# Performance work log

Hardware: AMD Instinct MI355X
Metric: run time of the kernel (lower is better)

Reference implementation:

```python
import jax, jax.numpy as jnp
import numpy as np

B, L, D, H, MLP = 8, 1024, 768, 12, 3072
DH = D // H
EPS = 1e-5


def setup_inputs() -> dict:
    key = jax.random.key(0)
    ks = jax.random.split(key, 8)
    s = 0.02
    return {
        "x": jax.random.normal(ks[0], (B, L, D), dtype=jnp.float32),
        "ln1_g": jnp.ones((D,), jnp.float32),
        "ln1_b": jnp.zeros((D,), jnp.float32),
        "w_qkv": jax.random.normal(ks[1], (3 * D, D), dtype=jnp.float32) * s,
        "w_out": jax.random.normal(ks[2], (D, D), dtype=jnp.float32) * s,
        "b_out": jnp.zeros((D,), jnp.float32),
        "ln2_g": jnp.ones((D,), jnp.float32),
        "ln2_b": jnp.zeros((D,), jnp.float32),
        "w1": jax.random.normal(ks[3], (MLP, D), dtype=jnp.float32) * s,
        "b1": jnp.zeros((MLP,), jnp.float32),
        "w2": jax.random.normal(ks[4], (D, MLP), dtype=jnp.float32) * s,
        "b2": jnp.zeros((D,), jnp.float32),
    }


def _layernorm(x, g, b):
    mu = jnp.mean(x, axis=-1, keepdims=True)
    var = jnp.mean(jnp.square(x - mu), axis=-1, keepdims=True)
    return (x - mu) * jax.lax.rsqrt(var + EPS) * g + b


def reference(x, ln1_g, ln1_b, w_qkv, w_out, b_out, ln2_g, ln2_b, w1, b1, w2, b2):
    # --- self-attention branch ---
    xn = _layernorm(x, ln1_g, ln1_b)                     # [B, L, D]
    qkv = jnp.einsum('bld,ed->ble', xn, w_qkv)           # [B, L, 3D]
    # rearrange 'b l (qkv h d) -> qkv b h l d'
    qkv = qkv.reshape(B, L, 3, H, DH).transpose(2, 0, 3, 1, 4)
    q, k, v = qkv[0], qkv[1], qkv[2]                     # [B, H, L, DH]
    scale = DH ** -0.5
    att = jnp.einsum('bhxd,bhyd->bhxy', q, k) * scale    # [B, H, L, L]
    att = jax.nn.softmax(att, axis=-1)
    o = jnp.einsum('bhxy,bhyd->bhxd', att, v)            # [B, H, L, DH]
    o = o.transpose(0, 2, 1, 3).reshape(B, L, D)         # 'b h l d -> b l (h d)'
    o = jnp.einsum('bld,ed->ble', o, w_out) + b_out
    x = x + o
    # --- MLP branch ---
    xn = _layernorm(x, ln2_g, ln2_b)
    h = jax.nn.gelu(jnp.einsum('bld,md->blm', xn, w1) + b1, approximate=False)
    h = jnp.einsum('blm,dm->bld', h, w2) + b2
    return x + h
```

## Files before the change

kernel.cpp:

```cpp
#include <hip/hip_runtime.h>
#include <hip/hip_bf16.h>
#include <math.h>

#define NB 8
#define NL 1024
#define ND 768
#define NH 12
#define NDH 64
#define NMLP 3072
#define NROWS 8192

typedef __attribute__((ext_vector_type(8))) short short8;
typedef __attribute__((ext_vector_type(8))) __bf16 bf16x8;
typedef __attribute__((ext_vector_type(4))) float f32x4;
typedef __attribute__((ext_vector_type(4))) float float4v;
typedef __attribute__((ext_vector_type(4))) unsigned short ushort4v;

__device__ __forceinline__ unsigned short f2b(float f) {
  unsigned u = __float_as_uint(f);
  unsigned r = (u + 0x7fffu + ((u >> 16) & 1u)) >> 16;
  return (unsigned short)r;
}

__device__ __forceinline__ f32x4 mfma16(short8 a, short8 b, f32x4 c) {
  return __builtin_amdgcn_mfma_f32_16x16x32_bf16(
      __builtin_bit_cast(bf16x8, a), __builtin_bit_cast(bf16x8, b), c, 0, 0, 0);
}

__device__ __forceinline__ void gl_lds16(const void* g, void* l) {
  __builtin_amdgcn_global_load_lds(
      (__attribute__((address_space(1))) void*)g,
      (__attribute__((address_space(3))) void*)l, 16, 0, 0);
}

__global__ __launch_bounds__(256) void cvt_all(const float* __restrict__ s0,
                                               const float* __restrict__ s1,
                                               const float* __restrict__ s2,
                                               const float* __restrict__ s3,
                                               unsigned short* __restrict__ d) {
  int i = (blockIdx.x * 256 + threadIdx.x) * 4;
  const float* s;
  int off;
  if (i < 1769472) { s = s0; off = i; }
  else if (i < 2359296) { s = s1; off = i - 1769472; }
  else if (i < 4718592) { s = s2; off = i - 2359296; }
  else { s = s3; off = i - 4718592; }
  float4v v = *(const float4v*)(s + off);
  ushort4v o;
  o[0] = f2b(v[0]); o[1] = f2b(v[1]); o[2] = f2b(v[2]); o[3] = f2b(v[3]);
  *(ushort4v*)(d + i) = o;
}

__global__ __launch_bounds__(256) void ln_bf16(const float* __restrict__ x,
                                               const float* __restrict__ g,
                                               const float* __restrict__ b,
                                               unsigned short* __restrict__ out) {
  int row = blockIdx.x, tid = threadIdx.x;
  const float* xr = x + (size_t)row * ND;
  float v0 = xr[tid], v1 = xr[tid + 256], v2 = xr[tid + 512];
  float s = v0 + v1 + v2;
  __shared__ float red[8];
#pragma unroll
  for (int o = 32; o > 0; o >>= 1) s += __shfl_down(s, o);
  int wv = tid >> 6, ln = tid & 63;
  if (ln == 0) red[wv] = s;
  __syncthreads();
  float mu = (red[0] + red[1] + red[2] + red[3]) * (1.0f / 768.0f);
  float d0 = v0 - mu, d1 = v1 - mu, d2 = v2 - mu;
  float q = d0 * d0 + d1 * d1 + d2 * d2;
#pragma unroll
  for (int o = 32; o > 0; o >>= 1) q += __shfl_down(q, o);
  if (ln == 0) red[4 + wv] = q;
  __syncthreads();
  float var = (red[4] + red[5] + red[6] + red[7]) * (1.0f / 768.0f);
  float rs = rsqrtf(var + 1e-5f);
  unsigned short* orow = out + (size_t)row * ND;
  orow[tid]       = f2b(d0 * rs * g[tid]       + b[tid]);
  orow[tid + 256] = f2b(d1 * rs * g[tid + 256] + b[tid + 256]);
  orow[tid + 512] = f2b(d2 * rs * g[tid + 512] + b[tid + 512]);
}

template <int MODE>
__global__ __launch_bounds__(256) void gemm_bt(
    const unsigned short* __restrict__ A, const unsigned short* __restrict__ W,
    unsigned short* __restrict__ outB, const float* __restrict__ bias,
    int M, int N, int K, int gx) {
  __shared__ __attribute__((aligned(16))) unsigned short As[3 * 4096];
  __shared__ __attribute__((aligned(16))) unsigned short Bs[3 * 4096];

  const int nwg = gridDim.x;
  const int bid = blockIdx.x;
  const int q = nwg >> 3, r = nwg & 7;
  const int xcd = bid & 7, idx = bid >> 3;
  const int swz = (xcd < r ? xcd * (q + 1) : r * (q + 1) + (xcd - r) * q) + idx;
  const int by = swz / gx, bx = swz - by * gx;
  const int m0 = by * 128, n0 = bx * 128;

  const int tid = threadIdx.x;
  const int wave = tid >> 6, lane = tid & 63;
  const int l15 = lane & 15, lhi = lane >> 4;
  const int wm = wave >> 1, wn = wave & 1;

  const int sr = tid >> 2, sc8 = (tid & 3) * 8;
  const unsigned short* Ag0 = A + (size_t)(m0 + sr) * K + sc8;
  const unsigned short* Ag1 = Ag0 + (size_t)64 * K;
  const unsigned short* Wg0 = W + (size_t)(n0 + sr) * K + sc8;
  const unsigned short* Wg1 = Wg0 + (size_t)64 * K;

  f32x4 acc[4][4];
#pragma unroll
  for (int i = 0; i < 4; i++)
#pragma unroll
    for (int j = 0; j < 4; j++) acc[i][j] = (f32x4){0.f, 0.f, 0.f, 0.f};

  auto STAGE = [&](int kelem, int buf) {
    unsigned short* Ad = As + buf * 4096 + wave * 512;
    unsigned short* Bd = Bs + buf * 4096 + wave * 512;
    gl_lds16(Ag0 + kelem, Ad);
    gl_lds16(Ag1 + kelem, Ad + 2048);
    gl_lds16(Wg0 + kelem, Bd);
    gl_lds16(Wg1 + kelem, Bd + 2048);
  };

  const int NT = K >> 5;
  STAGE(0, 0);
  STAGE(32, 1);

  int cb = 0, nbuf = 2;
  for (int t = 0; t < NT; ++t) {
    if (t + 2 < NT) {
      STAGE((t + 2) * 32, nbuf);
      asm volatile("s_waitcnt vmcnt(8)" ::: "memory");
    } else if (t + 2 == NT) {
      asm volatile("s_waitcnt vmcnt(4)" ::: "memory");
    } else {
      asm volatile("s_waitcnt vmcnt(0)" ::: "memory");
    }
    __builtin_amdgcn_s_barrier();

    const unsigned short* Ac = As + cb * 4096;
    const unsigned short* Bc = Bs + cb * 4096;
    short8 af[4], bf[4];
#pragma unroll
    for (int i = 0; i < 4; i++)
      af[i] = *(const short8*)&Ac[(wm * 64 + i * 16 + l15) * 32 + lhi * 8];
#pragma unroll
    for (int j = 0; j < 4; j++)
      bf[j] = *(const short8*)&Bc[(wn * 64 + j * 16 + l15) * 32 + lhi * 8];
#pragma unroll
    for (int i = 0; i < 4; i++)
#pragma unroll
      for (int j = 0; j < 4; j++) acc[i][j] = mfma16(af[i], bf[j], acc[i][j]);

    asm volatile("s_waitcnt lgkmcnt(0)" ::: "memory");
    __builtin_amdgcn_s_barrier();
    cb = (cb == 2) ? 0 : cb + 1;
    nbuf = (nbuf == 2) ? 0 : nbuf + 1;
  }

#pragma unroll
  for (int i = 0; i < 4; i++) {
    int row = m0 + wm * 64 + i * 16 + lhi * 4;
#pragma unroll
    for (int j = 0; j < 4; j++) {
      int col = n0 + wn * 64 + j * 16 + l15;
#pragma unroll
      for (int r2 = 0; r2 < 4; r2++) {
        float v = acc[i][j][r2];
        size_t idxo = (size_t)(row + r2) * N + col;
        if (MODE == 0) {
          outB[idxo] = f2b(v);
        } else {
          float t2 = v + bias[col];
          float z = 1.5957691f * t2 * (1.0f + 0.044715f * t2 * t2);
          float e = __expf(-z);
          outB[idxo] = f2b(__fdividef(t2, 1.0f + e));
        }
      }
    }
  }
}

template <int MODE>
__global__ __launch_bounds__(256) void gemm_bt64(
    const unsigned short* __restrict__ A, const unsigned short* __restrict__ W,
    float* __restrict__ outF, const float* __restrict__ bias,
    const float* __restrict__ resid, int M, int N, int K, int gx) {
  __shared__ __attribute__((aligned(16))) unsigned short As[2 * 4096];
  __shared__ __attribute__((aligned(16))) unsigned short Bs[2 * 8192];

  const int nwg = gridDim.x;
  const int bid = blockIdx.x;
  const int q = nwg >> 3, r = nwg & 7;
  const int xcd = bid & 7, idx = bid >> 3;
  const int swz = (xcd < r ? xcd * (q + 1) : r * (q + 1) + (xcd - r) * q) + idx;
  const int by = swz / gx, bx = swz - by * gx;
  const int m0 = by * 64, n0 = bx * 128;

  const int tid = threadIdx.x;
  const int wave = tid >> 6, lane = tid & 63;
  const int l15 = lane & 15, lhi = lane >> 4;
  const int wn = wave;

  const int sr = tid >> 3;
  const int swc8 = ((tid & 7) ^ (sr & 7)) * 8;
  const unsigned short* Aga = A + (size_t)(m0 + sr) * K + swc8;
  const unsigned short* Wga = W + (size_t)(n0 + sr) * K + swc8;

  f32x4 acc[4][2];
#pragma unroll
  for (int i = 0; i < 4; i++)
#pragma unroll
    for (int j = 0; j < 2; j++) acc[i][j] = (f32x4){0.f, 0.f, 0.f, 0.f};

  auto STAGE = [&](int kelem, int buf) {
    unsigned short* Ad = As + buf * 4096 + wave * 512;
    unsigned short* Bd = Bs + buf * 8192 + wave * 512;
    gl_lds16(Aga + kelem, Ad);
    gl_lds16(Aga + (size_t)32 * K + kelem, Ad + 2048);
    gl_lds16(Wga + kelem, Bd);
    gl_lds16(Wga + (size_t)32 * K + kelem, Bd + 2048);
    gl_lds16(Wga + (size_t)64 * K + kelem, Bd + 4096);
    gl_lds16(Wga + (size_t)96 * K + kelem, Bd + 6144);
  };

  const int NT = K >> 6;
  STAGE(0, 0);

  for (int t = 0; t < NT; ++t) {
    const int cb = t & 1;
    if (t + 1 < NT) {
      STAGE((t + 1) * 64, cb ^ 1);
      asm volatile("s_waitcnt vmcnt(6)" ::: "memory");
    } else {
      asm volatile("s_waitcnt vmcnt(0)" ::: "memory");
    }
    __builtin_amdgcn_s_barrier();

    const unsigned short* Ac = As + cb * 4096;
    const unsigned short* Bc = Bs + cb * 8192;
    short8 af[4][2], bf[2][2];
#pragma unroll
    for (int i = 0; i < 4; i++) {
      int ar = i * 16 + l15;
#pragma unroll
      for (int kk = 0; kk < 2; kk++)
        af[i][kk] = *(const short8*)&Ac[ar * 64 + (((kk * 4 + lhi) ^ (ar & 7)) * 8)];
    }
#pragma unroll
    for (int j = 0; j < 2; j++) {
      int br = wn * 32 + j * 16 + l15;
#pragma unroll
      for (int kk = 0; kk < 2; kk++)
        bf[j][kk] = *(const short8*)&Bc[br * 64 + (((kk * 4 + lhi) ^ (br & 7)) * 8)];
    }
#pragma unroll
    for (int kk = 0; kk < 2; kk++)
#pragma unroll
      for (int i = 0; i < 4; i++)
#pragma unroll
        for (int j = 0; j < 2; j++)
          acc[i][j] = mfma16(af[i][kk], bf[j][kk], acc[i][j]);

    asm volatile("s_waitcnt lgkmcnt(0)" ::: "memory");
    __builtin_amdgcn_s_barrier();
  }

#pragma unroll
  for (int i = 0; i < 4; i++) {
    int row = m0 + i * 16 + lhi * 4;
#pragma unroll
    for (int j = 0; j < 2; j++) {
      int col = n0 + wn * 32 + j * 16 + l15;
#pragma unroll
      for (int r2 = 0; r2 < 4; r2++) {
        size_t idxo = (size_t)(row + r2) * N + col;
        outF[idxo] = acc[i][j][r2] + bias[col] + resid[idxo];
      }
    }
  }
}

__global__ __launch_bounds__(256) void vtrans(const unsigned short* __restrict__ qkv,
                                              unsigned short* __restrict__ vT) {
  int bid = blockIdx.x;
  int tt = bid & 15;
  int t2 = bid >> 4;
  int h = t2 % NH, b = t2 / NH;
  __shared__ unsigned short L[64 * 72];
  int t = threadIdx.x;
  int row0 = t >> 3;
  int col8 = (t & 7) * 8;
#pragma unroll
  for (int s = 0; s < 2; s++) {
    int row = row0 + s * 32;
    const unsigned short* src =
        qkv + ((size_t)(b * NL + tt * 64 + row)) * 2304 + 1536 + h * 64 + col8;
    short8 v = *(const short8*)src;
    int wchunk = row >> 3;
#pragma unroll
    for (int j = 0; j < 8; j++) {
      int d = col8 + j;
      int cp = wchunk ^ (d >> 3);
      L[d * 72 + cp * 8 + (row & 7)] = (unsigned short)v[j];
    }
  }
  __syncthreads();
#pragma unroll
  for (int s = 0; s < 2; s++) {
    int d = (t >> 3) + s * 32;
    int rc = t & 7;
    int cp = rc ^ (d >> 3);
    short8 ov = *(const short8*)&L[d * 72 + cp * 8];
    *(short8*)(vT + ((size_t)((b * NH + h) * 64 + d)) * NL + tt * 64 + rc * 8) = ov;
  }
}

#define L2E8 0.180336880f
__global__ __launch_bounds__(256, 3) void attn_kernel(
    const unsigned short* __restrict__ qkv, const unsigned short* __restrict__ vT,
    unsigned short* __restrict__ o) {
  int bid0 = blockIdx.x;
  int lb = (bid0 & 7) * 96 + (bid0 >> 3);
  int qt = lb & 7;
  int t = lb >> 3;
  int h = t % NH, b = t / NH;
  const int tid = threadIdx.x;
  const int wave = tid >> 6, lane = tid & 63;
  const int l15 = lane & 15, lhi = lane >> 4;
  const int sw = l15 & 7;
  __shared__ __attribute__((aligned(16))) unsigned short Ks[2 * 64 * 64];
  __shared__ __attribute__((aligned(16))) unsigned short Vs[2 * 64 * 64];
  __shared__ __attribute__((aligned(16))) unsigned short Ps[2 * 4 * 16 * 64];

  const unsigned short* qp = qkv + (size_t)(b * NL + qt * 128) * 2304 + h * 64;
  short8 qf[2][2];
#pragma unroll
  for (int i = 0; i < 2; i++)
#pragma unroll
    for (int kk = 0; kk < 2; kk++)
      qf[i][kk] = *(const short8*)(qp + (size_t)(i * 64 + wave * 16 + l15) * 2304 +
                                   kk * 32 + lhi * 8);

  const int srow = tid >> 3, scpos = tid & 7;
  const int sc8 = (scpos ^ (srow & 7)) * 8;
  const unsigned short* ks0 =
      qkv + (size_t)(b * NL + srow) * 2304 + 768 + h * 64 + sc8;
  const unsigned short* vt0 =
      vT + (size_t)((b * NH + h) * 64 + srow) * NL + sc8;
  unsigned short* Pw0 = Ps + wave * 1024;
  unsigned short* Pw1 = Ps + 4096 + wave * 1024;

  int paddr[4][4];
#pragma unroll
  for (int kb = 0; kb < 4; kb++) {
    int ch = kb * 2 + (l15 >> 3);
#pragma unroll
    for (int r = 0; r < 4; r++) {
      int row = lhi * 4 + r;
      paddr[kb][r] = row * 64 + ((ch ^ (row & 7)) << 3) + sw;
    }
  }

  f32x4 acc[2][4];
  f32x4 accL[2];
#pragma unroll
  for (int i = 0; i < 2; i++) {
    accL[i] = (f32x4){0.f, 0.f, 0.f, 0.f};
#pragma unroll
    for (int nb = 0; nb < 4; nb++) acc[i][nb] = (f32x4){0.f, 0.f, 0.f, 0.f};
  }

  short8 onesf;
#pragma unroll
  for (int j = 0; j < 8; j++) onesf[j] = (short)0x3F80;

#define STAGE(ktile, buf)                                                    \
  {                                                                          \
    const unsigned short* ksrc = ks0 + (size_t)((ktile) * 64) * 2304;        \
    const unsigned short* vsrc = vt0 + (ktile) * 64;                         \
    unsigned short* kb_ = Ks + (buf) * 4096 + wave * 512;                    \
    unsigned short* vb_ = Vs + (buf) * 4096 + wave * 512;                    \
    gl_lds16(ksrc, kb_);                                                     \
    gl_lds16(ksrc + (size_t)32 * 2304, kb_ + 2048);                          \
    gl_lds16(vsrc, vb_);                                                     \
    gl_lds16(vsrc + 32 * NL, vb_ + 2048);                                    \
  }

  STAGE(0, 0);

  for (int kt = 0; kt < 16; kt++) {
    const int cb = kt & 1;
    if (kt + 1 < 16) {
      STAGE(kt + 1, cb ^ 1);
      asm volatile("s_waitcnt vmcnt(4)" ::: "memory");
    } else {
      asm volatile("s_waitcnt vmcnt(0)" ::: "memory");
    }
    __builtin_amdgcn_s_barrier();

    const unsigned short* Kc = Ks + cb * 4096;
    const unsigned short* Vc = Vs + cb * 4096;

    f32x4 sv[2][4];
    __builtin_amdgcn_s_setprio(1);
#pragma unroll
    for (int kb = 0; kb < 4; kb++) {
      short8 kf0 = *(const short8*)&Kc[(kb * 16 + l15) * 64 + (lhi ^ sw) * 8];
      short8 kf1 = *(const short8*)&Kc[(kb * 16 + l15) * 64 + ((4 + lhi) ^ sw) * 8];
#pragma unroll
      for (int i = 0; i < 2; i++) {
        f32x4 s = mfma16(qf[i][0], kf0, (f32x4){0.f, 0.f, 0.f, 0.f});
        sv[i][kb] = mfma16(qf[i][1], kf1, s);
      }
    }
    __builtin_amdgcn_s_setprio(0);

    short8 vf[4][2];
#pragma unroll
    for (int nb = 0; nb < 4; nb++)
#pragma unroll
      for (int kk = 0; kk < 2; kk++)
        vf[nb][kk] =
            *(const short8*)&Vc[(nb * 16 + l15) * 64 + ((kk * 4 + lhi) ^ sw) * 8];

#pragma unroll
    for (int i = 0; i < 2; i++) {
      unsigned short* Pw = i ? Pw1 : Pw0;
#pragma unroll
      for (int kb = 0; kb < 4; kb++)
#pragma unroll
        for (int r = 0; r < 4; r++) {
          float p = exp2f(sv[i][kb][r] * L2E8);
          Pw[paddr[kb][r]] = (unsigned short)(__float_as_uint(p) >> 16);
        }
    }

    __builtin_amdgcn_s_setprio(1);
#pragma unroll
    for (int i = 0; i < 2; i++) {
      const unsigned short* Pw = i ? Pw1 : Pw0;
      short8 pf0 = *(const short8*)&Pw[l15 * 64 + (lhi ^ sw) * 8];
      short8 pf1 = *(const short8*)&Pw[l15 * 64 + ((4 + lhi) ^ sw) * 8];
#pragma unroll
      for (int nb = 0; nb < 4; nb++) {
        acc[i][nb] = mfma16(pf0, vf[nb][0], acc[i][nb]);
        acc[i][nb] = mfma16(pf1, vf[nb][1], acc[i][nb]);
      }
      accL[i] = mfma16(pf0, onesf, accL[i]);
      accL[i] = mfma16(pf1, onesf, accL[i]);
    }
    __builtin_amdgcn_s_setprio(0);
    __builtin_amdgcn_s_barrier();
  }
#undef STAGE

#pragma unroll
  for (int i = 0; i < 2; i++) {
    float inv[4];
#pragma unroll
    for (int r = 0; r < 4; r++) inv[r] = 1.0f / accL[i][r];
    size_t obase =
        (size_t)(b * NL + qt * 128 + i * 64 + wave * 16 + lhi * 4) * ND + h * 64;
#pragma unroll
    for (int nb = 0; nb < 4; nb++)
#pragma unroll
      for (int r = 0; r < 4; r++)
        o[obase + (size_t)r * ND + nb * 16 + l15] = f2b(acc[i][nb][r] * inv[r]);
  }
}

extern "C" void kernel_launch(void* const* d_in, const int* in_sizes, int n_in,
                              void* d_out, int out_size, void* d_ws, size_t ws_size,
                              hipStream_t stream) {
  const float* x     = (const float*)d_in[0];
  const float* ln1_g = (const float*)d_in[1];
  const float* ln1_b = (const float*)d_in[2];
  const float* w_qkv = (const float*)d_in[3];
  const float* w_out = (const float*)d_in[4];
  const float* b_out = (const float*)d_in[5];
  const float* ln2_g = (const float*)d_in[6];
  const float* ln2_b = (const float*)d_in[7];
  const float* w1    = (const float*)d_in[8];
  const float* b1    = (const float*)d_in[9];
  const float* w2    = (const float*)d_in[10];
  const float* b2    = (const float*)d_in[11];
  float* out = (float*)d_out;

  char* p = (char*)d_ws;
  unsigned short* wqkv_b = (unsigned short*)p; p += (size_t)2304 * 768 * 2;
  unsigned short* wout_b = (unsigned short*)p; p += (size_t)768 * 768 * 2;
  unsigned short* w1_b   = (unsigned short*)p; p += (size_t)3072 * 768 * 2;
  unsigned short* w2_b   = (unsigned short*)p; p += (size_t)768 * 3072 * 2;
  unsigned short* xn     = (unsigned short*)p; p += (size_t)NROWS * ND * 2;
  unsigned short* qkvb   = (unsigned short*)p; p += (size_t)NROWS * NMLP * 2;
  float* x1 = (float*)p;  p += (size_t)NROWS * ND * 4;
  unsigned short* vTb = (unsigned short*)x1;

  cvt_all<<<7077888 / 4 / 256, 256, 0, stream>>>(w_qkv, w_out, w1, w2, wqkv_b);

  ln_bf16<<<NROWS, 256, 0, stream>>>(x, ln1_g, ln1_b, xn);
  gemm_bt<0><<<1152, 256, 0, stream>>>(
      xn, wqkv_b, qkvb, nullptr, NROWS, 2304, 768, 18);
  vtrans<<<NB * NH * (NL / 64), 256, 0, stream>>>(qkvb, vTb);
  attn_kernel<<<NB * NH * (NL / 128), 256, 0, stream>>>(qkvb, vTb, xn);
  gemm_bt64<1><<<768, 256, 0, stream>>>(
      xn, wout_b, x1, b_out, x, NROWS, 768, 768, 6);
  ln_bf16<<<NROWS, 256, 0, stream>>>(x1, ln2_g, ln2_b, xn);
  gemm_bt<2><<<1536, 256, 0, stream>>>(
      xn, w1_b, qkvb, b1, NROWS, 3072, 768, 24);
  gemm_bt64<3><<<768, 256, 0, stream>>>(
      qkvb, w2_b, out, b2, x1, NROWS, 768, 3072, 6);
}
```

Before: 256.2 us.

## Rework 128x128 GEMM to 512 threads, BK=64, double buffering and XOR-swizzled LDS

The 128x128-tile GEMM used for the QKV and MLP-up projections now runs with 8 waves instead of 4, each computing a 64x32 sub-tile. The K step grows from 32 to 64, the pipeline drops from triple to double buffering, and the LDS layout uses an XOR swizzle to avoid bank conflicts on the wider rows. The aim is more waves to hide latency, fewer barriers per K, and conflict-free fragment loads. The trade-off is less prefetch depth and a larger LDS footprint per block.

```diff
diff --git a/kernel.cpp b/kernel.cpp
--- a/kernel.cpp
+++ b/kernel.cpp
@@ -81,12 +81,12 @@
 }
 
 template <int MODE>
-__global__ __launch_bounds__(256) void gemm_bt(
+__global__ __launch_bounds__(512) void gemm128(
     const unsigned short* __restrict__ A, const unsigned short* __restrict__ W,
     unsigned short* __restrict__ outB, const float* __restrict__ bias,
     int M, int N, int K, int gx) {
-  __shared__ __attribute__((aligned(16))) unsigned short As[3 * 4096];
-  __shared__ __attribute__((aligned(16))) unsigned short Bs[3 * 4096];
+  __shared__ __attribute__((aligned(16))) unsigned short As[2 * 8192];
+  __shared__ __attribute__((aligned(16))) unsigned short Bs[2 * 8192];
 
   const int nwg = gridDim.x;
   const int bid = blockIdx.x;
@@ -99,71 +99,77 @@
   const int tid = threadIdx.x;
   const int wave = tid >> 6, lane = tid & 63;
   const int l15 = lane & 15, lhi = lane >> 4;
-  const int wm = wave >> 1, wn = wave & 1;
-
-  const int sr = tid >> 2, sc8 = (tid & 3) * 8;
-  const unsigned short* Ag0 = A + (size_t)(m0 + sr) * K + sc8;
-  const unsigned short* Ag1 = Ag0 + (size_t)64 * K;
-  const unsigned short* Wg0 = W + (size_t)(n0 + sr) * K + sc8;
-  const unsigned short* Wg1 = Wg0 + (size_t)64 * K;
-
-  f32x4 acc[4][4];
+  const int sw = l15 & 7;
+  const int wm = wave >> 2, wn = wave & 3;
+
+  const int sr = tid >> 3;
+  const int swc8 = ((tid & 7) ^ (sr & 7)) * 8;
+  const unsigned short* Aga = A + (size_t)(m0 + sr) * K + swc8;
+  const unsigned short* Wga = W + (size_t)(n0 + sr) * K + swc8;
+
+  f32x4 acc[4][2];
 #pragma unroll
   for (int i = 0; i < 4; i++)
 #pragma unroll
-    for (int j = 0; j < 4; j++) acc[i][j] = (f32x4){0.f, 0.f, 0.f, 0.f};
+    for (int j = 0; j < 2; j++) acc[i][j] = (f32x4){0.f, 0.f, 0.f, 0.f};
 
   auto STAGE = [&](int kelem, int buf) {
-    unsigned short* Ad = As + buf * 4096 + wave * 512;
-    unsigned short* Bd = Bs + buf * 4096 + wave * 512;
-    gl_lds16(Ag0 + kelem, Ad);
-    gl_lds16(Ag1 + kelem, Ad + 2048);
-    gl_lds16(Wg0 + kelem, Bd);
-    gl_lds16(Wg1 + kelem, Bd + 2048);
+    unsigned short* Ad = As + buf * 8192 + wave * 512;
+    unsigned short* Bd = Bs + buf * 8192 + wave * 512;
+    gl_lds16(Aga + kelem, Ad);
+    gl_lds16(Aga + (size_t)64 * K + kelem, Ad + 4096);
+    gl_lds16(Wga + kelem, Bd);
+    gl_lds16(Wga + (size_t)64 * K + kelem, Bd + 4096);
   };
 
-  const int NT = K >> 5;
+  const int NT = K >> 6;
   STAGE(0, 0);
-  STAGE(32, 1);
-
-  int cb = 0, nbuf = 2;
+
   for (int t = 0; t < NT; ++t) {
-    if (t + 2 < NT) {
-      STAGE((t + 2) * 32, nbuf);
-      asm volatile("s_waitcnt vmcnt(8)" ::: "memory");
-    } else if (t + 2 == NT) {
+    const int cb = t & 1;
+    if (t + 1 < NT) {
+      STAGE((t + 1) * 64, cb ^ 1);
       asm volatile("s_waitcnt vmcnt(4)" ::: "memory");
     } else {
       asm volatile("s_waitcnt vmcnt(0)" ::: "memory");
     }
     __builtin_amdgcn_s_barrier();
 
-    const unsigned short* Ac = As + cb * 4096;
-    const unsigned short* Bc = Bs + cb * 4096;
-    short8 af[4], bf[4];
-#pragma unroll
-    for (int i = 0; i < 4; i++)
-      af[i] = *(const short8*)&Ac[(wm * 64 + i * 16 + l15) * 32 + lhi * 8];
-#pragma unroll
-    for (int j = 0; j < 4; j++)
-      bf[j] = *(const short8*)&Bc[(wn * 64 + j * 16 + l15) * 32 + lhi * 8];
-#pragma unroll
-    for (int i = 0; i < 4; i++)
-#pragma unroll
-      for (int j = 0; j < 4; j++) acc[i][j] = mfma16(af[i], bf[j], acc[i][j]);
+    const unsigned short* Ac = As + cb * 8192;
+    const unsigned short* Bc = Bs + cb * 8192;
+    short8 af[4][2], bf[2][2];
+#pragma unroll
+    for (int i = 0; i < 4; i++) {
+      int ar = wm * 64 + i * 16 + l15;
+#pragma unroll
+      for (int kk = 0; kk < 2; kk++)
+        af[i][kk] = *(const short8*)&Ac[ar * 64 + (((kk * 4 + lhi) ^ sw) * 8)];
+    }
+#pragma unroll
+    for (int j = 0; j < 2; j++) {
+      int br = wn * 32 + j * 16 + l15;
+#pragma unroll
+      for (int kk = 0; kk < 2; kk++)
+        bf[j][kk] = *(const short8*)&Bc[br * 64 + (((kk * 4 + lhi) ^ sw) * 8)];
+    }
+#pragma unroll
+    for (int kk = 0; kk < 2; kk++)
+#pragma unroll
+      for (int i = 0; i < 4; i++)
+#pragma unroll
+        for (int j = 0; j < 2; j++)
+          acc[i][j] = mfma16(af[i][kk], bf[j][kk], acc[i][j]);
 
     asm volatile("s_waitcnt lgkmcnt(0)" ::: "memory");
     __builtin_amdgcn_s_barrier();
-    cb = (cb == 2) ? 0 : cb + 1;
-    nbuf = (nbuf == 2) ? 0 : nbuf + 1;
   }
 
 #pragma unroll
   for (int i = 0; i < 4; i++) {
     int row = m0 + wm * 64 + i * 16 + lhi * 4;
 #pragma unroll
-    for (int j = 0; j < 4; j++) {
-      int col = n0 + wn * 64 + j * 16 + l15;
+    for (int j = 0; j < 2; j++) {
+      int col = n0 + wn * 32 + j * 16 + l15;
 #pragma unroll
       for (int r2 = 0; r2 < 4; r2++) {
         float v = acc[i][j][r2];
@@ -182,7 +188,7 @@
 }
 
 template <int MODE>
-__global__ __launch_bounds__(256) void gemm_bt64(
+__global__ __launch_bounds__(256) void gemm64(
     const unsigned short* __restrict__ A, const unsigned short* __restrict__ W,
     float* __restrict__ outF, const float* __restrict__ bias,
     const float* __restrict__ resid, int M, int N, int K, int gx) {
@@ -500,15 +506,15 @@
   cvt_all<<<7077888 / 4 / 256, 256, 0, stream>>>(w_qkv, w_out, w1, w2, wqkv_b);
 
   ln_bf16<<<NROWS, 256, 0, stream>>>(x, ln1_g, ln1_b, xn);
-  gemm_bt<0><<<1152, 256, 0, stream>>>(
+  gemm128<0><<<1152, 512, 0, stream>>>(
       xn, wqkv_b, qkvb, nullptr, NROWS, 2304, 768, 18);
   vtrans<<<NB * NH * (NL / 64), 256, 0, stream>>>(qkvb, vTb);
   attn_kernel<<<NB * NH * (NL / 128), 256, 0, stream>>>(qkvb, vTb, xn);
-  gemm_bt64<1><<<768, 256, 0, stream>>>(
+  gemm64<1><<<768, 256, 0, stream>>>(
       xn, wout_b, x1, b_out, x, NROWS, 768, 768, 6);
   ln_bf16<<<NROWS, 256, 0, stream>>>(x1, ln2_g, ln2_b, xn);
-  gemm_bt<2><<<1536, 256, 0, stream>>>(
+  gemm128<2><<<1536, 512, 0, stream>>>(
       xn, w1_b, qkvb, b1, NROWS, 3072, 768, 24);
-  gemm_bt64<3><<<768, 256, 0, stream>>>(
+  gemm64<3><<<768, 256, 0, stream>>>(
       qkvb, w2_b, out, b2, x1, NROWS, 768, 3072, 6);
 }
```

New measurement: 249.3 us, median of 2. -2.7%, faster.
